# Performance work log

Hardware: AMD Instinct MI355X
Metric: run time of the kernel (lower is better)

## Reference

```python
import jax, jax.numpy as jnp
import numpy as np

ATOM_FDIM = 35
BOND_FDIM = 5
MAX_NB = 15
HIDDEN = 512
DEPTH = 6
N_MOLS = 1024
ATOMS_PER_MOL = 32
N_ATOMS = N_MOLS * ATOMS_PER_MOL      # 32768
N_BONDS = 2 * N_ATOMS                  # 65536 (each bond appears in both directions)
N_MESS = 8192                          # tree messages (row 0 is the zero pad slot)
TOTAL_MSG = N_MESS + N_BONDS           # index space for agraph/bgraph


def setup_inputs() -> dict:
    key = jax.random.key(0)
    ks = jax.random.split(key, 8)
    fatoms = jax.random.normal(ks[0], (N_ATOMS, ATOM_FDIM), jnp.float32)
    fbonds = jax.random.normal(ks[1], (N_BONDS, ATOM_FDIM + BOND_FDIM), jnp.float32)
    agraph = jax.random.randint(ks[2], (N_ATOMS, MAX_NB), 0, TOTAL_MSG, dtype=jnp.int32)
    bgraph = jax.random.randint(ks[3], (N_BONDS, MAX_NB), 0, TOTAL_MSG, dtype=jnp.int32)
    # row 0 of the concatenated message table is the padding slot -> zero it
    tree_message = jax.random.normal(ks[4], (N_MESS, HIDDEN), jnp.float32).at[0].set(0.0)
    starts = jnp.arange(N_MOLS, dtype=jnp.int32) * ATOMS_PER_MOL
    scope = jnp.stack([starts, jnp.full((N_MOLS,), ATOMS_PER_MOL, jnp.int32)], axis=1)
    s_i = 1.0 / np.sqrt(ATOM_FDIM + BOND_FDIM)
    s_h = 1.0 / np.sqrt(HIDDEN)
    s_o = 1.0 / np.sqrt(ATOM_FDIM + HIDDEN)
    W_i = jax.random.normal(ks[5], (ATOM_FDIM + BOND_FDIM, HIDDEN), jnp.float32) * s_i
    W_h = jax.random.normal(ks[6], (HIDDEN, HIDDEN), jnp.float32) * s_h
    W_o = jax.random.normal(ks[7], (ATOM_FDIM + HIDDEN, HIDDEN), jnp.float32) * s_o
    b_o = jnp.zeros((HIDDEN,), jnp.float32)
    return {"fatoms": fatoms, "fbonds": fbonds, "agraph": agraph, "bgraph": bgraph,
            "scope": scope, "tree_message": tree_message,
            "W_i": W_i, "W_h": W_h, "W_o": W_o, "b_o": b_o}


def reference(fatoms, fbonds, agraph, bgraph, scope, tree_message, W_i, W_h, W_o, b_o):
    binput = fbonds @ W_i                         # [B, H]
    graph_message = jax.nn.relu(binput)

    def step(gm, _):
        message = jnp.concatenate([tree_message, gm], axis=0)   # [M+B, H]
        nei = message[bgraph].sum(axis=1)                       # gather-sum [B, H]
        return jax.nn.relu(binput + nei @ W_h), None

    graph_message, _ = jax.lax.scan(step, graph_message, None, length=DEPTH - 1)

    message = jnp.concatenate([tree_message, graph_message], axis=0)
    nei = message[agraph].sum(axis=1)             # [A, H]
    ainput = jnp.concatenate([fatoms, nei], axis=1)
    atom_hiddens = jax.nn.relu(ainput @ W_o + b_o)

    # scope is uniform (st = i*ATOMS_PER_MOL, le = ATOMS_PER_MOL) -> static segment ids
    seg = jnp.repeat(jnp.arange(N_MOLS), ATOMS_PER_MOL)
    sums = jax.ops.segment_sum(atom_hiddens, seg, num_segments=N_MOLS)
    return sums / scope[:, 1:].astype(atom_hiddens.dtype)
```

## Files before the change

kernel.cpp:

```cpp
#include <hip/hip_runtime.h>
#include <stdint.h>


#define MAX_NB 15
#define HID 512
#define NA 32768
#define NB 65536
#define NMESS 8192

typedef unsigned short u16;
typedef unsigned int u32;
typedef __bf16 bf16x8 __attribute__((ext_vector_type(8)));
typedef float f32x4 __attribute__((ext_vector_type(4)));

__device__ __forceinline__ u16 f2bf(float f) {
  u32 u = __builtin_bit_cast(u32, f);
  u32 r = (u + 0x7fffu + ((u >> 16) & 1u)) >> 16;
  return (u16)r;
}
__device__ __forceinline__ float bf2f(u16 b) {
  u32 u = ((u32)b) << 16;
  return __builtin_bit_cast(float, u);
}
__device__ __forceinline__ float bflo(u32 u) {
  return __builtin_bit_cast(float, u << 16);
}
__device__ __forceinline__ float bfhi(u32 u) {
  return __builtin_bit_cast(float, u & 0xffff0000u);
}

__device__ __forceinline__ void async16(const u16* g, u16* l) {
  __builtin_amdgcn_global_load_lds(
      (const __attribute__((address_space(1))) u32*)g,
      (__attribute__((address_space(3))) u32*)l, 16, 0, 0);
}

__global__ __launch_bounds__(256) void prep_kernel(
    const float* __restrict__ fbonds, const float* __restrict__ tree,
    const float* __restrict__ Wi, const float* __restrict__ Wh,
    const float* __restrict__ Wo, u16* __restrict__ msg,
    u16* __restrict__ fbpad, u16* __restrict__ wi_t, u16* __restrict__ wh_t,
    u16* __restrict__ wo_t) {
  int t = blockIdx.x * 256 + threadIdx.x;
  const int N0 = NMESS * HID;
  const int N1 = NB * 64;
  const int N2 = 512 * 64;
  const int N3 = 512 * 512;
  const int N4 = 512 * 576;
  if (t < N0) { msg[t] = f2bf(tree[t]); return; }
  t -= N0;
  if (t < N1) {
    int row = t >> 6, c = t & 63;
    fbpad[t] = (c < 40) ? f2bf(fbonds[row * 40 + c]) : (u16)0;
    return;
  }
  t -= N1;
  if (t < N2) {
    int n = t >> 6, k = t & 63;
    wi_t[t] = (k < 40) ? f2bf(Wi[k * 512 + n]) : (u16)0;
    return;
  }
  t -= N2;
  if (t < N3) {
    int n = t >> 9, k = t & 511;
    wh_t[t] = f2bf(Wh[k * 512 + n]);
    return;
  }
  t -= N3;
  if (t < N4) {
    int n = t / 576, k = t - n * 576;
    float v = 0.f;
    if (k < 512) v = Wo[(35 + k) * 512 + n];
    else if (k < 547) v = Wo[(k - 512) * 512 + n];
    wo_t[t] = f2bf(v);
    return;
  }
}

template <int ATOMS>
__global__ __launch_bounds__(256) void gather_dma(
    const u16* __restrict__ msg, const int* __restrict__ graph,
    const float* __restrict__ fatoms, u16* __restrict__ outbuf) {
  __shared__ __align__(16) u16 sbuf[4][8][HID];
  const int lane = threadIdx.x & 63;
  const int w = threadIdx.x >> 6;
  u16* buf = &sbuf[w][0][0];
  const int rowBase = (blockIdx.x * 4 + w) * 4;
  const int OSTRIDE = ATOMS ? 576 : HID;

  for (int r = 0; r < 4; r++) {
    const int row = rowBase + r;
    const int* idxp = graph + row * MAX_NB;
    int myid = (lane < MAX_NB) ? idxp[lane] : 0;
    int ids[MAX_NB];
#pragma unroll
    for (int j = 0; j < MAX_NB; j++) ids[j] = __shfl(myid, j, 64);

    float acc[8] = {0, 0, 0, 0, 0, 0, 0, 0};
    __builtin_amdgcn_s_waitcnt(0);
#pragma unroll
    for (int j = 0; j < 8; j++)
      async16(msg + (size_t)ids[j] * HID + lane * 8, buf + j * HID + lane * 8);
    __builtin_amdgcn_s_waitcnt(0);
#pragma unroll
    for (int j = 0; j < 8; j++) {
      uint4 v = *(const uint4*)(buf + j * HID + lane * 8);
      acc[0] += bflo(v.x); acc[1] += bfhi(v.x);
      acc[2] += bflo(v.y); acc[3] += bfhi(v.y);
      acc[4] += bflo(v.z); acc[5] += bfhi(v.z);
      acc[6] += bflo(v.w); acc[7] += bfhi(v.w);
    }
    __builtin_amdgcn_s_waitcnt(0);
#pragma unroll
    for (int j = 8; j < MAX_NB; j++)
      async16(msg + (size_t)ids[j] * HID + lane * 8,
              buf + (j - 8) * HID + lane * 8);
    __builtin_amdgcn_s_waitcnt(0);
#pragma unroll
    for (int j = 8; j < MAX_NB; j++) {
      uint4 v = *(const uint4*)(buf + (j - 8) * HID + lane * 8);
      acc[0] += bflo(v.x); acc[1] += bfhi(v.x);
      acc[2] += bflo(v.y); acc[3] += bfhi(v.y);
      acc[4] += bflo(v.z); acc[5] += bfhi(v.z);
      acc[6] += bflo(v.w); acc[7] += bfhi(v.w);
    }
    uint4 o;
    o.x = (u32)f2bf(acc[0]) | ((u32)f2bf(acc[1]) << 16);
    o.y = (u32)f2bf(acc[2]) | ((u32)f2bf(acc[3]) << 16);
    o.z = (u32)f2bf(acc[4]) | ((u32)f2bf(acc[5]) << 16);
    o.w = (u32)f2bf(acc[6]) | ((u32)f2bf(acc[7]) << 16);
    u16* orow = outbuf + (size_t)row * OSTRIDE;
    *(uint4*)(orow + lane * 8) = o;
    if (ATOMS) {
      float tv = (lane < 35) ? fatoms[(size_t)row * 35 + lane] : 0.f;
      orow[512 + lane] = f2bf(tv);
    }
  }
}

template <int EPI>
__global__ __launch_bounds__(256) void gemm_k(
    const u16* __restrict__ A, const u16* __restrict__ Bt, int K, int mtx,
    u16* __restrict__ binput, u16* __restrict__ msgout,
    const float* __restrict__ bo, const int* __restrict__ scope,
    float* __restrict__ out) {
  __shared__ __align__(16) u16 As[128 * 32];
  __shared__ __align__(16) u16 Bs[128 * 32];
  const int L = blockIdx.x;
  const int xcd = L & 7;
  const int q = L >> 3;
  const int mBase = (xcd * mtx + (q >> 2)) * 128;
  const int nBase = (q & 3) * 128;
  const int t = threadIdx.x;
  const int lane = t & 63;
  const int w = t >> 6;
  const int wm = w & 1, wn = w >> 1;
  const int r = t >> 2;
  const int c8 = (t & 3) * 8;
  const int q8 = (lane >> 4) * 8;
  const int l15 = lane & 15;

  f32x4 acc[4][4];
#pragma unroll
  for (int i = 0; i < 4; i++)
#pragma unroll
    for (int j = 0; j < 4; j++)
#pragma unroll
      for (int rg = 0; rg < 4; rg++) acc[i][j][rg] = 0.f;

  for (int kb = 0; kb < K; kb += 32) {
    __syncthreads();
    async16(A + (size_t)(mBase + r) * K + kb + c8, As + r * 32 + c8);
    async16(A + (size_t)(mBase + r + 64) * K + kb + c8, As + (r + 64) * 32 + c8);
    async16(Bt + (size_t)(nBase + r) * K + kb + c8, Bs + r * 32 + c8);
    async16(Bt + (size_t)(nBase + r + 64) * K + kb + c8, Bs + (r + 64) * 32 + c8);
    __syncthreads();
    bf16x8 av[4], bv[4];
#pragma unroll
    for (int i = 0; i < 4; i++)
      av[i] = *(const bf16x8*)(As + (wm * 64 + i * 16 + l15) * 32 + q8);
#pragma unroll
    for (int j = 0; j < 4; j++)
      bv[j] = *(const bf16x8*)(Bs + (wn * 64 + j * 16 + l15) * 32 + q8);
#pragma unroll
    for (int i = 0; i < 4; i++)
#pragma unroll
      for (int j = 0; j < 4; j++)
        acc[i][j] = __builtin_amdgcn_mfma_f32_16x16x32_bf16(av[i], bv[j],
                                                            acc[i][j], 0, 0, 0);
  }

  if (EPI == 2) {
#pragma unroll
    for (int m = 0; m < 2; m++) {
      int mol = (mBase + wm * 64 + m * 32) >> 5;
      float inv_le = 1.0f / (float)scope[mol * 2 + 1];
#pragma unroll
      for (int j = 0; j < 4; j++) {
        int col = nBase + wn * 64 + j * 16 + l15;
        float bias = bo[col];
        float s = 0.f;
#pragma unroll
        for (int i = 2 * m; i < 2 * m + 2; i++)
#pragma unroll
          for (int rg = 0; rg < 4; rg++)
            s += fmaxf(acc[i][j][rg] + bias, 0.f);
        s += __shfl_xor(s, 16, 64);
        s += __shfl_xor(s, 32, 64);
        if (lane < 16) out[(size_t)mol * HID + col] = s * inv_le;
      }
    }
  } else {
#pragma unroll
    for (int i = 0; i < 4; i++) {
      int row = mBase + wm * 64 + i * 16 + (lane >> 4) * 4;
#pragma unroll
      for (int j = 0; j < 4; j++) {
        int col = nBase + wn * 64 + j * 16 + l15;
#pragma unroll
        for (int rg = 0; rg < 4; rg++) {
          float v = acc[i][j][rg];
          size_t gi = (size_t)(row + rg) * HID + col;
          if (EPI == 0) {
            binput[gi] = f2bf(v);
            msgout[gi + (size_t)NMESS * HID] = f2bf(fmaxf(v, 0.f));
          } else {
            v += bf2f(binput[gi]);
            msgout[gi + (size_t)NMESS * HID] = f2bf(fmaxf(v, 0.f));
          }
        }
      }
    }
  }
}

extern "C" void kernel_launch(void* const* d_in, const int* in_sizes, int n_in,
                              void* d_out, int out_size, void* d_ws,
                              size_t ws_size, hipStream_t stream) {
  const float* fatoms = (const float*)d_in[0];
  const float* fbonds = (const float*)d_in[1];
  const int* agraph = (const int*)d_in[2];
  const int* bgraph = (const int*)d_in[3];
  const int* scope = (const int*)d_in[4];
  const float* tree = (const float*)d_in[5];
  const float* Wi = (const float*)d_in[6];
  const float* Wh = (const float*)d_in[7];
  const float* Wo = (const float*)d_in[8];
  const float* bo = (const float*)d_in[9];
  float* out = (float*)d_out;

  char* ws = (char*)d_ws;
  u16* msg = (u16*)(ws);
  u16* binput = (u16*)(ws + 75497472ull);
  u16* nei = (u16*)(ws + 142606336ull);
  u16* wi_t = (u16*)(ws + 209715200ull);
  u16* wh_t = (u16*)(ws + 209780736ull);
  u16* wo_t = (u16*)(ws + 210305024ull);
  u16* fbpad = nei;
  u16* ainput = binput;

  prep_kernel<<<35072, 256, 0, stream>>>(fbonds, tree, Wi, Wh, Wo, msg, fbpad,
                                         wi_t, wh_t, wo_t);

  gemm_k<0><<<2048, 256, 0, stream>>>(fbpad, wi_t, 64, 64, binput, msg,
                                      nullptr, nullptr, nullptr);
  for (int d = 0; d < 5; d++) {
    gather_dma<0><<<NB / 16, 256, 0, stream>>>(msg, bgraph, nullptr, nei);
    gemm_k<1><<<2048, 256, 0, stream>>>(nei, wh_t, 512, 64, binput, msg,
                                        nullptr, nullptr, nullptr);
  }
  gather_dma<1><<<NA / 16, 256, 0, stream>>>(msg, agraph, fatoms, ainput);
  gemm_k<2><<<1024, 256, 0, stream>>>(ainput, wo_t, 576, 32, nullptr, nullptr,
                                      bo, scope, out);
}
```

Before: 1.274 ms.

## Sort gather indices per wave and accumulate eight rows in registers

```diff
diff --git a/kernel.cpp b/kernel.cpp
--- a/kernel.cpp
+++ b/kernel.cpp
@@ -77,62 +77,87 @@
   }
 }
 
+#define ACC8(S)                                                       \
+  {                                                                   \
+    acc[S * 8 + 0] += bflo(v.x); acc[S * 8 + 1] += bfhi(v.x);         \
+    acc[S * 8 + 2] += bflo(v.y); acc[S * 8 + 3] += bfhi(v.y);         \
+    acc[S * 8 + 4] += bflo(v.z); acc[S * 8 + 5] += bfhi(v.z);         \
+    acc[S * 8 + 6] += bflo(v.w); acc[S * 8 + 7] += bfhi(v.w);         \
+  }
+
 template <int ATOMS>
-__global__ __launch_bounds__(256) void gather_dma(
+__global__ __launch_bounds__(256) void gather_sorted(
     const u16* __restrict__ msg, const int* __restrict__ graph,
     const float* __restrict__ fatoms, u16* __restrict__ outbuf) {
-  __shared__ __align__(16) u16 sbuf[4][8][HID];
+  __shared__ u32 sk[4][128];
   const int lane = threadIdx.x & 63;
   const int w = threadIdx.x >> 6;
-  u16* buf = &sbuf[w][0][0];
-  const int rowBase = (blockIdx.x * 4 + w) * 4;
+  u32* mysk = sk[w];
+  const int rowBase = (blockIdx.x * 4 + w) * 8;
   const int OSTRIDE = ATOMS ? 576 : HID;
-
-  for (int r = 0; r < 4; r++) {
-    const int row = rowBase + r;
-    const int* idxp = graph + row * MAX_NB;
-    int myid = (lane < MAX_NB) ? idxp[lane] : 0;
-    int ids[MAX_NB];
-#pragma unroll
-    for (int j = 0; j < MAX_NB; j++) ids[j] = __shfl(myid, j, 64);
-
-    float acc[8] = {0, 0, 0, 0, 0, 0, 0, 0};
-    __builtin_amdgcn_s_waitcnt(0);
-#pragma unroll
-    for (int j = 0; j < 8; j++)
-      async16(msg + (size_t)ids[j] * HID + lane * 8, buf + j * HID + lane * 8);
-    __builtin_amdgcn_s_waitcnt(0);
-#pragma unroll
-    for (int j = 0; j < 8; j++) {
-      uint4 v = *(const uint4*)(buf + j * HID + lane * 8);
-      acc[0] += bflo(v.x); acc[1] += bfhi(v.x);
-      acc[2] += bflo(v.y); acc[3] += bfhi(v.y);
-      acc[4] += bflo(v.z); acc[5] += bfhi(v.z);
-      acc[6] += bflo(v.w); acc[7] += bfhi(v.w);
-    }
-    __builtin_amdgcn_s_waitcnt(0);
-#pragma unroll
-    for (int j = 8; j < MAX_NB; j++)
-      async16(msg + (size_t)ids[j] * HID + lane * 8,
-              buf + (j - 8) * HID + lane * 8);
-    __builtin_amdgcn_s_waitcnt(0);
-#pragma unroll
-    for (int j = 8; j < MAX_NB; j++) {
-      uint4 v = *(const uint4*)(buf + (j - 8) * HID + lane * 8);
-      acc[0] += bflo(v.x); acc[1] += bfhi(v.x);
-      acc[2] += bflo(v.y); acc[3] += bfhi(v.y);
-      acc[4] += bflo(v.z); acc[5] += bfhi(v.z);
-      acc[6] += bflo(v.w); acc[7] += bfhi(v.w);
-    }
+  const int* gp = graph + rowBase * MAX_NB;
+
+  {
+    int r0 = lane;
+    u32 k0 = ((u32)gp[r0] << 3) | ((u32)(r0 * 2185) >> 15);
+    mysk[r0] = k0;
+    int r1 = lane + 64;
+    u32 k1 = (r1 < 120) ? (((u32)gp[r1] << 3) | ((u32)(r1 * 2185) >> 15)) : 0u;
+    mysk[r1] = k1;
+  }
+
+  for (int k = 2; k <= 128; k <<= 1) {
+    for (int j = k >> 1; j > 0; j >>= 1) {
+      __syncthreads();
+      int i = ((lane & ~(j - 1)) << 1) | (lane & (j - 1));
+      int h = i | j;
+      u32 a = mysk[i], b = mysk[h];
+      bool up = ((i & k) == 0);
+      if ((a > b) == up) { mysk[i] = b; mysk[h] = a; }
+    }
+  }
+  __syncthreads();
+
+  float acc[64];
+#pragma unroll
+  for (int i = 0; i < 64; i++) acc[i] = 0.f;
+
+  for (int e = 0; e < 128; e += 4) {
+    int kk[4];
+    uint4 vv[4];
+#pragma unroll
+    for (int q = 0; q < 4; q++)
+      kk[q] = __builtin_amdgcn_readfirstlane((int)mysk[e + q]);
+#pragma unroll
+    for (int q = 0; q < 4; q++)
+      vv[q] = *(const uint4*)(msg + (size_t)((u32)kk[q] >> 3) * HID + lane * 8);
+#pragma unroll
+    for (int q = 0; q < 4; q++) {
+      uint4 v = vv[q];
+      switch (kk[q] & 7) {
+        case 0: ACC8(0); break;
+        case 1: ACC8(1); break;
+        case 2: ACC8(2); break;
+        case 3: ACC8(3); break;
+        case 4: ACC8(4); break;
+        case 5: ACC8(5); break;
+        case 6: ACC8(6); break;
+        case 7: ACC8(7); break;
+      }
+    }
+  }
+
+#pragma unroll
+  for (int s = 0; s < 8; s++) {
     uint4 o;
-    o.x = (u32)f2bf(acc[0]) | ((u32)f2bf(acc[1]) << 16);
-    o.y = (u32)f2bf(acc[2]) | ((u32)f2bf(acc[3]) << 16);
-    o.z = (u32)f2bf(acc[4]) | ((u32)f2bf(acc[5]) << 16);
-    o.w = (u32)f2bf(acc[6]) | ((u32)f2bf(acc[7]) << 16);
-    u16* orow = outbuf + (size_t)row * OSTRIDE;
+    o.x = (u32)f2bf(acc[s * 8 + 0]) | ((u32)f2bf(acc[s * 8 + 1]) << 16);
+    o.y = (u32)f2bf(acc[s * 8 + 2]) | ((u32)f2bf(acc[s * 8 + 3]) << 16);
+    o.z = (u32)f2bf(acc[s * 8 + 4]) | ((u32)f2bf(acc[s * 8 + 5]) << 16);
+    o.w = (u32)f2bf(acc[s * 8 + 6]) | ((u32)f2bf(acc[s * 8 + 7]) << 16);
+    u16* orow = outbuf + (size_t)(rowBase + s) * OSTRIDE;
     *(uint4*)(orow + lane * 8) = o;
     if (ATOMS) {
-      float tv = (lane < 35) ? fatoms[(size_t)row * 35 + lane] : 0.f;
+      float tv = (lane < 35) ? fatoms[(size_t)(rowBase + s) * 35 + lane] : 0.f;
       orow[512 + lane] = f2bf(tv);
     }
   }
@@ -265,11 +290,11 @@
   gemm_k<0><<<2048, 256, 0, stream>>>(fbpad, wi_t, 64, 64, binput, msg,
                                       nullptr, nullptr, nullptr);
   for (int d = 0; d < 5; d++) {
-    gather_dma<0><<<NB / 16, 256, 0, stream>>>(msg, bgraph, nullptr, nei);
+    gather_sorted<0><<<NB / 32, 256, 0, stream>>>(msg, bgraph, nullptr, nei);
     gemm_k<1><<<2048, 256, 0, stream>>>(nei, wh_t, 512, 64, binput, msg,
                                         nullptr, nullptr, nullptr);
   }
-  gather_dma<1><<<NA / 16, 256, 0, stream>>>(msg, agraph, fatoms, ainput);
+  gather_sorted<1><<<NA / 32, 256, 0, stream>>>(msg, agraph, fatoms, ainput);
   gemm_k<2><<<1024, 256, 0, stream>>>(ainput, wo_t, 576, 32, nullptr, nullptr,
                                       bo, scope, out);
 }
```

Result: slower. 1.476 ms (+15.8%).
